# Kernel optimization log

Hardware: AMD Instinct MI355X
Metric: run time of the kernel (lower is better)

Reference implementation:

```python
import jax, jax.numpy as jnp
import numpy as np

GROUP_SIZE = 128
QMAX = 127.0  # int8 symmetric: 2^(8-1) - 1
EPS = 1e-8


def group_quant_dequant(t, group_size=GROUP_SIZE):
    """Group-wise symmetric int8 fake-quantize along the last dim.

    Groups of `group_size` along the last axis share one scale
    s = max|t| / 127; values are rounded/clipped to int8 range and
    immediately dequantized (q * s), which is the exact math of a
    group-quantized GEMM with inline dequantization.
    """
    shape = t.shape
    g = t.reshape(shape[:-1] + (shape[-1] // group_size, group_size))
    s = jnp.maximum(jnp.max(jnp.abs(g), axis=-1, keepdims=True) / QMAX, EPS)
    q = jnp.clip(jnp.round(g / s), -QMAX, QMAX)
    return (q * s).reshape(shape)


def setup_inputs() -> dict:
    key = jax.random.key(0)
    k0, k1, k2, k3 = jax.random.split(key, 4)
    B, S, H, I = 2, 2048, 4096, 11008
    x = jax.random.normal(k0, (B, S, H), dtype=jnp.float32)
    # Linear weights stored [out_features, in_features]; quant groups run
    # along the in_features (contraction) axis.
    w_gate = jax.random.normal(k1, (I, H), dtype=jnp.float32) * (1.0 / np.sqrt(H))
    w_up = jax.random.normal(k2, (I, H), dtype=jnp.float32) * (1.0 / np.sqrt(H))
    w_down = jax.random.normal(k3, (H, I), dtype=jnp.float32) * (1.0 / np.sqrt(I))
    return {"x": x, "w_gate": w_gate, "w_up": w_up, "w_down": w_down}


def reference(x, w_gate, w_up, w_down):
    # quantize input activations (QuantTensor(x))
    xq = group_quant_dequant(x)
    # gate/up quant-GEMMs with inline weight dequant
    gate = jnp.einsum('bsh,ih->bsi', xq, group_quant_dequant(w_gate))
    up = jnp.einsum('bsh,ih->bsi', xq, group_quant_dequant(w_up))
    # SwiGLU: SiLU(gate) * up, then requantize the hidden activation
    hidden = jax.nn.silu(gate) * up
    hq = group_quant_dequant(hidden)
    # down quant-GEMM -> dequantized float output
    out = jnp.einsum('bsi,hi->bsh', hq, group_quant_dequant(w_down))
    return out
```

## Files before the change

### kernel.cpp

```cpp
#include <hip/hip_runtime.h>
#include <math.h>

typedef int i32x4 __attribute__((ext_vector_type(4)));
typedef float f32x4 __attribute__((ext_vector_type(4)));
typedef float f32x2 __attribute__((ext_vector_type(2)));

#define QMAXF 127.0f
#define EPSQ 1e-8f

__device__ __forceinline__ void gl_lds16(const void* g, void* l) {
  __builtin_amdgcn_global_load_lds(
      (const __attribute__((address_space(1))) unsigned int*)g,
      (__attribute__((address_space(3))) unsigned int*)l, 16, 0, 0);
}
__device__ __forceinline__ void gl_lds4(const void* g, void* l) {
  __builtin_amdgcn_global_load_lds(
      (const __attribute__((address_space(1))) unsigned int*)g,
      (__attribute__((address_space(3))) unsigned int*)l, 4, 0, 0);
}

__global__ __launch_bounds__(256)
void qdq8(const float* __restrict__ in, char* __restrict__ q,
          float* __restrict__ sT, long n_groups, int gpr, int R) {
  long wid = (long)blockIdx.x * 4 + (threadIdx.x >> 6);
  if (wid >= n_groups) return;
  int lane = threadIdx.x & 63;
  long base = wid * 128 + lane * 2;
  f32x2 v = *(const f32x2*)(in + base);
  float m = fmaxf(fabsf(v.x), fabsf(v.y));
#pragma unroll
  for (int off = 32; off; off >>= 1) m = fmaxf(m, __shfl_xor(m, off));
  float s = fmaxf(m / QMAXF, EPSQ);
  int q0 = (int)fminf(fmaxf(rintf(v.x / s), -QMAXF), QMAXF);
  int q1 = (int)fminf(fmaxf(rintf(v.y / s), -QMAXF), QMAXF);
  *(unsigned short*)(q + base) =
      (unsigned short)((q0 & 0xff) | ((q1 & 0xff) << 8));
  if (lane == 0) {
    long row = wid / gpr;
    long gc = wid - row * gpr;
    sT[gc * (long)R + row] = s;
  }
}


__global__ __launch_bounds__(256, 2)
void gemm_gu_i8(const char* __restrict__ Aq, const char* __restrict__ Bg,
                const char* __restrict__ Bu,
                const float* __restrict__ sAT, const float* __restrict__ sGT,
                const float* __restrict__ sUT,
                char* __restrict__ Hq, float* __restrict__ sHT,
                int M, int N, int K, int NBN) {
  __shared__ char sA[16384];
  __shared__ char sBG[16384];
  __shared__ char sBU[16384];
  __shared__ float sSa[128], sSg[128], sSu[128];
  __shared__ float rmx[2][128];
  __shared__ float rs[128];

  const int tid = threadIdx.x;
  const int lane = tid & 63;
  const int wid = tid >> 6;
  const int wr = (wid >> 1) * 64;
  const int wc = (wid & 1) * 64;
  const int l15 = lane & 15, l16 = lane >> 4;

  const int nwg = gridDim.x;
  const int wg = ((int)blockIdx.x & 7) * (nwg >> 3) + ((int)blockIdx.x >> 3);
  const long m0 = (long)(wg / NBN) * 128;
  const long n0 = (long)(wg % NBN) * 128;

  const char* gA[4];
  const char* gG[4];
  const char* gU[4];
#pragma unroll
  for (int k = 0; k < 4; k++) {
    int c = tid + 256 * k;
    long row = c >> 3;
    int off = ((c & 7) * 16) ^ ((int)(row & 7) << 4);
    gA[k] = Aq + (m0 + row) * K + off;
    gG[k] = Bg + (n0 + row) * K + off;
    gU[k] = Bu + (n0 + row) * K + off;
  }

  const int rdSwz = (l15 & 7) << 4;
  const int colK0 = (l16 * 16) ^ rdSwz;
  const int colK1 = (64 + l16 * 16) ^ rdSwz;

  f32x4 accg[4][4], accu[4][4];
#pragma unroll
  for (int i = 0; i < 4; i++)
#pragma unroll
    for (int j = 0; j < 4; j++) {
      accg[i][j] = (f32x4){0.f, 0.f, 0.f, 0.f};
      accu[i][j] = (f32x4){0.f, 0.f, 0.f, 0.f};
    }
  const i32x4 iz = {0, 0, 0, 0};

  const int KG = K >> 7;
  for (int g = 0; g < KG; ++g) {
    const long kb = (long)g << 7;
#pragma unroll
    for (int k = 0; k < 4; k++) {
      gl_lds16(gA[k] + kb, &sA[(tid + 256 * k) * 16]);
      gl_lds16(gG[k] + kb, &sBG[(tid + 256 * k) * 16]);
      gl_lds16(gU[k] + kb, &sBU[(tid + 256 * k) * 16]);
    }
    if (wid < 2) {
      gl_lds4(sAT + (long)g * M + m0 + tid, &sSa[wid * 64]);
      gl_lds4(sUT + (long)g * N + n0 + tid, &sSu[wid * 64]);
    } else {
      gl_lds4(sGT + (long)g * N + n0 + (tid - 128), &sSg[(wid - 2) * 64]);
    }
    __syncthreads();

    i32x4 af[4][2];
#pragma unroll
    for (int i = 0; i < 4; i++) {
      const int rb = (wr + i * 16 + l15) * 128;
      af[i][0] = *(const i32x4*)&sA[rb + colK0];
      af[i][1] = *(const i32x4*)&sA[rb + colK1];
    }
    f32x4 sa4[4];
#pragma unroll
    for (int i = 0; i < 4; i++)
      sa4[i] = *(const f32x4*)&sSa[wr + i * 16 + l16 * 4];

#pragma unroll
    for (int j = 0; j < 4; j++) {
      const int rbB = (wc + j * 16 + l15) * 128;
      i32x4 bgf[2], buf_[2];
      bgf[0] = *(const i32x4*)&sBG[rbB + colK0];
      bgf[1] = *(const i32x4*)&sBG[rbB + colK1];
      buf_[0] = *(const i32x4*)&sBU[rbB + colK0];
      buf_[1] = *(const i32x4*)&sBU[rbB + colK1];
      float sbg = sSg[wc + j * 16 + l15];
      float sbu = sSu[wc + j * 16 + l15];
#pragma unroll
      for (int i = 0; i < 4; i++) {
        i32x4 tg = __builtin_amdgcn_mfma_i32_16x16x64_i8(af[i][0], bgf[0], iz, 0, 0, 0);
        tg = __builtin_amdgcn_mfma_i32_16x16x64_i8(af[i][1], bgf[1], tg, 0, 0, 0);
        i32x4 tu = __builtin_amdgcn_mfma_i32_16x16x64_i8(af[i][0], buf_[0], iz, 0, 0, 0);
        tu = __builtin_amdgcn_mfma_i32_16x16x64_i8(af[i][1], buf_[1], tu, 0, 0, 0);
        f32x4 mg = sa4[i] * sbg;
        f32x4 mu = sa4[i] * sbu;
        accg[i][j] += mg * __builtin_convertvector(tg, f32x4);
        accu[i][j] += mu * __builtin_convertvector(tu, f32x4);
      }
    }
    __syncthreads();
  }

  float pm[4][4];
#pragma unroll
  for (int i = 0; i < 4; i++)
#pragma unroll
    for (int r = 0; r < 4; r++) pm[i][r] = 0.f;
#pragma unroll
  for (int i = 0; i < 4; i++)
#pragma unroll
    for (int j = 0; j < 4; j++)
#pragma unroll
      for (int r = 0; r < 4; r++) {
        float gv = accg[i][j][r];
        float h = gv / (1.f + expf(-gv)) * accu[i][j][r];
        accu[i][j][r] = h;
        pm[i][r] = fmaxf(pm[i][r], fabsf(h));
      }
#pragma unroll
  for (int i = 0; i < 4; i++)
#pragma unroll
    for (int r = 0; r < 4; r++) {
      pm[i][r] = fmaxf(pm[i][r], __shfl_xor(pm[i][r], 1));
      pm[i][r] = fmaxf(pm[i][r], __shfl_xor(pm[i][r], 2));
      pm[i][r] = fmaxf(pm[i][r], __shfl_xor(pm[i][r], 4));
      pm[i][r] = fmaxf(pm[i][r], __shfl_xor(pm[i][r], 8));
    }
#pragma unroll
  for (int i = 0; i < 4; i++)
#pragma unroll
    for (int r = 0; r < 4; r++)
      if (l15 == i * 4 + r) rmx[wid & 1][wr + i * 16 + l16 * 4 + r] = pm[i][r];
  __syncthreads();
  if (tid < 128) {
    float mx = fmaxf(rmx[0][tid], rmx[1][tid]);
    float s = fmaxf(mx / QMAXF, EPSQ);
    rs[tid] = s;
    sHT[(n0 >> 7) * (long)M + m0 + tid] = s;
  }
  __syncthreads();
#pragma unroll
  for (int i = 0; i < 4; i++) {
    f32x4 sr = *(const f32x4*)&rs[wr + i * 16 + l16 * 4];
#pragma unroll
    for (int j = 0; j < 4; j++)
#pragma unroll
      for (int r = 0; r < 4; r++) {
        float qv = fminf(fmaxf(rintf(accu[i][j][r] / sr[r]), -QMAXF), QMAXF);
        sA[(wr + i * 16 + l16 * 4 + r) * 128 + wc + j * 16 + l15] = (char)(int)qv;
      }
  }
  __syncthreads();
  {
    int row = tid >> 1, seg = tid & 1;
    const i32x4* src = (const i32x4*)&sA[row * 128 + seg * 64];
    i32x4* dst = (i32x4*)(Hq + (m0 + row) * N + n0 + seg * 64);
#pragma unroll
    for (int k = 0; k < 4; k++) dst[k] = src[k];
  }
}

__global__ __launch_bounds__(256, 2)
void gemm_dn_i8(const char* __restrict__ Aq, const char* __restrict__ Bq,
                const float* __restrict__ sAT, const float* __restrict__ sBT,
                float* __restrict__ C, int M, int N, int K, int NBN) {
  __shared__ char sA[16384];
  __shared__ char sB[16384];
  __shared__ float sSa[128], sSb[128];

  const int tid = threadIdx.x;
  const int lane = tid & 63;
  const int wid = tid >> 6;
  const int wr = (wid >> 1) * 64;
  const int wc = (wid & 1) * 64;
  const int l15 = lane & 15, l16 = lane >> 4;

  const int nwg = gridDim.x;
  const int wg = ((int)blockIdx.x & 7) * (nwg >> 3) + ((int)blockIdx.x >> 3);
  const long m0 = (long)(wg / NBN) * 128;
  const long n0 = (long)(wg % NBN) * 128;

  const char* gA[4];
  const char* gB[4];
#pragma unroll
  for (int k = 0; k < 4; k++) {
    int c = tid + 256 * k;
    long row = c >> 3;
    int off = ((c & 7) * 16) ^ ((int)(row & 7) << 4);
    gA[k] = Aq + (m0 + row) * K + off;
    gB[k] = Bq + (n0 + row) * K + off;
  }

  const int rdSwz = (l15 & 7) << 4;
  const int colK0 = (l16 * 16) ^ rdSwz;
  const int colK1 = (64 + l16 * 16) ^ rdSwz;

  f32x4 acc[4][4];
#pragma unroll
  for (int i = 0; i < 4; i++)
#pragma unroll
    for (int j = 0; j < 4; j++) acc[i][j] = (f32x4){0.f, 0.f, 0.f, 0.f};
  const i32x4 iz = {0, 0, 0, 0};

  const int KG = K >> 7;
  for (int g = 0; g < KG; ++g) {
    const long kb = (long)g << 7;
#pragma unroll
    for (int k = 0; k < 4; k++) {
      gl_lds16(gA[k] + kb, &sA[(tid + 256 * k) * 16]);
      gl_lds16(gB[k] + kb, &sB[(tid + 256 * k) * 16]);
    }
    if (wid < 2) {
      gl_lds4(sAT + (long)g * M + m0 + tid, &sSa[wid * 64]);
    } else {
      gl_lds4(sBT + (long)g * N + n0 + (tid - 128), &sSb[(wid - 2) * 64]);
    }
    __syncthreads();

    i32x4 af[4][2];
#pragma unroll
    for (int i = 0; i < 4; i++) {
      const int rb = (wr + i * 16 + l15) * 128;
      af[i][0] = *(const i32x4*)&sA[rb + colK0];
      af[i][1] = *(const i32x4*)&sA[rb + colK1];
    }
    f32x4 sa4[4];
#pragma unroll
    for (int i = 0; i < 4; i++)
      sa4[i] = *(const f32x4*)&sSa[wr + i * 16 + l16 * 4];

#pragma unroll
    for (int j = 0; j < 4; j++) {
      const int rbB = (wc + j * 16 + l15) * 128;
      i32x4 bf[2];
      bf[0] = *(const i32x4*)&sB[rbB + colK0];
      bf[1] = *(const i32x4*)&sB[rbB + colK1];
      float sb = sSb[wc + j * 16 + l15];
#pragma unroll
      for (int i = 0; i < 4; i++) {
        i32x4 t = __builtin_amdgcn_mfma_i32_16x16x64_i8(af[i][0], bf[0], iz, 0, 0, 0);
        t = __builtin_amdgcn_mfma_i32_16x16x64_i8(af[i][1], bf[1], t, 0, 0, 0);
        f32x4 ms = sa4[i] * sb;
        acc[i][j] += ms * __builtin_convertvector(t, f32x4);
      }
    }
    __syncthreads();
  }

#pragma unroll
  for (int i = 0; i < 4; i++)
#pragma unroll
    for (int j = 0; j < 4; j++)
#pragma unroll
      for (int r = 0; r < 4; r++) {
        long row = m0 + wr + i * 16 + l16 * 4 + r;
        long col = n0 + wc + j * 16 + l15;
        C[row * N + col] = acc[i][j][r];
      }
}

extern "C" void kernel_launch(void* const* d_in, const int* in_sizes, int n_in,
                              void* d_out, int out_size, void* d_ws, size_t ws_size,
                              hipStream_t stream) {
  (void)n_in; (void)out_size;
  const float* x  = (const float*)d_in[0];
  const float* wg = (const float*)d_in[1];
  const float* wu = (const float*)d_in[2];
  const float* wd = (const float*)d_in[3];
  float* out = (float*)d_out;

  const long H = 4096;
  const long M = in_sizes[0] / H;
  const long I = in_sizes[1] / H;
  const long GH = H >> 7;
  const long GI = I >> 7;

  char* ws = (char*)d_ws;
  size_t off = 0;
  char* xq  = ws + off; off += (size_t)(M * H);
  char* wgq = ws + off; off += (size_t)(I * H);
  char* wuq = ws + off; off += (size_t)(I * H);
  char* wdq = ws + off; off += (size_t)(H * I);
  char* hq  = ws + off; off += (size_t)(M * I);
  float* s_x = (float*)(ws + off); off += (size_t)(GH * M) * 4;
  float* s_g = (float*)(ws + off); off += (size_t)(GH * I) * 4;
  float* s_u = (float*)(ws + off); off += (size_t)(GH * I) * 4;
  float* s_d = (float*)(ws + off); off += (size_t)(GI * H) * 4;
  float* s_h = (float*)(ws + off); off += (size_t)(GI * M) * 4;
  if (ws_size < off) return;

  {
    long ng;
    ng = M * H / 128;
    qdq8<<<dim3((unsigned)((ng + 3) / 4)), dim3(256), 0, stream>>>(x, xq, s_x, ng, (int)GH, (int)M);
    ng = I * H / 128;
    qdq8<<<dim3((unsigned)((ng + 3) / 4)), dim3(256), 0, stream>>>(wg, wgq, s_g, ng, (int)GH, (int)I);
    qdq8<<<dim3((unsigned)((ng + 3) / 4)), dim3(256), 0, stream>>>(wu, wuq, s_u, ng, (int)GH, (int)I);
    ng = H * I / 128;
    qdq8<<<dim3((unsigned)((ng + 3) / 4)), dim3(256), 0, stream>>>(wd, wdq, s_d, ng, (int)GI, (int)H);
  }

  {
    const int NBN = (int)GI;
    const int grid = (int)(M / 128) * NBN;
    gemm_gu_i8<<<dim3(grid), dim3(256), 0, stream>>>(
        xq, wgq, wuq, s_x, s_g, s_u, hq, s_h, (int)M, (int)I, (int)H, NBN);
  }
  {
    const int NBN = (int)GH;
    const int grid = (int)(M / 128) * NBN;
    gemm_dn_i8<<<dim3(grid), dim3(256), 0, stream>>>(
        hq, wdq, s_h, s_d, out, (int)M, (int)H, (int)I, NBN);
  }
}
```

Measured before the change: 1.172 ms.

## Prefetch next K-tile into LDS during MFMA compute in int8 GEMMs

Restructures both int8 GEMM main loops so the next K-group's global-to-LDS loads are issued right after the current fragments are read into registers. The MFMA work then overlaps with those loads, and the gate/up kernel splits the B loads so the up-weight tile is refetched only after its fragments have been consumed. Launch bounds drop to one block per SIMD to leave room for the larger register-resident fragments. The cost is lower occupancy and extra barriers per iteration.

```diff
diff --git a/kernel.cpp b/kernel.cpp
--- a/kernel.cpp
+++ b/kernel.cpp
@@ -43,7 +43,7 @@
 }
 
 
-__global__ __launch_bounds__(256, 2)
+__global__ __launch_bounds__(256, 1)
 void gemm_gu_i8(const char* __restrict__ Aq, const char* __restrict__ Bg,
                 const char* __restrict__ Bu,
                 const float* __restrict__ sAT, const float* __restrict__ sGT,
@@ -69,17 +69,24 @@
   const long m0 = (long)(wg / NBN) * 128;
   const long n0 = (long)(wg % NBN) * 128;
 
-  const char* gA[4];
-  const char* gG[4];
-  const char* gU[4];
-#pragma unroll
-  for (int k = 0; k < 4; k++) {
-    int c = tid + 256 * k;
-    long row = c >> 3;
-    int off = ((c & 7) * 16) ^ ((int)(row & 7) << 4);
-    gA[k] = Aq + (m0 + row) * K + off;
-    gG[k] = Bg + (n0 + row) * K + off;
-    gU[k] = Bu + (n0 + row) * K + off;
+  const long row0 = tid >> 3;
+  const int off0 = (((tid & 7) * 16)) ^ ((int)(row0 & 7) << 4);
+  const long kstr = 32L * K;
+  const char* gA0 = Aq + (m0 + row0) * K + off0;
+  const char* gG0 = Bg + (n0 + row0) * K + off0;
+  const char* gU0 = Bu + (n0 + row0) * K + off0;
+
+  const float* pS0;
+  const float* pS1;
+  float* dS0;
+  float* dS1;
+  long st0 = 0, st1 = 0;
+  if (wid < 2) {
+    pS0 = sAT + m0 + tid; dS0 = &sSa[wid * 64]; st0 = M;
+    pS1 = sUT + n0 + tid; dS1 = &sSu[wid * 64]; st1 = N;
+  } else {
+    pS0 = sGT + n0 + (tid - 128); dS0 = &sSg[(wid - 2) * 64]; st0 = N;
+    pS1 = pS0; dS1 = dS0;
   }
 
   const int rdSwz = (l15 & 7) << 4;
@@ -95,58 +102,87 @@
       accu[i][j] = (f32x4){0.f, 0.f, 0.f, 0.f};
     }
   const i32x4 iz = {0, 0, 0, 0};
-
   const int KG = K >> 7;
+
+#pragma unroll
+  for (int k = 0; k < 4; k++) {
+    gl_lds16(gA0 + k * kstr, &sA[tid * 16 + k * 4096]);
+    gl_lds16(gG0 + k * kstr, &sBG[tid * 16 + k * 4096]);
+    gl_lds16(gU0 + k * kstr, &sBU[tid * 16 + k * 4096]);
+  }
+  gA0 += 128; gG0 += 128; gU0 += 128;
+  gl_lds4(pS0, dS0); pS0 += st0;
+  if (wid < 2) { gl_lds4(pS1, dS1); pS1 += st1; }
+  asm volatile("s_waitcnt vmcnt(0)" ::: "memory");
+  __syncthreads();
+
   for (int g = 0; g < KG; ++g) {
-    const long kb = (long)g << 7;
-#pragma unroll
-    for (int k = 0; k < 4; k++) {
-      gl_lds16(gA[k] + kb, &sA[(tid + 256 * k) * 16]);
-      gl_lds16(gG[k] + kb, &sBG[(tid + 256 * k) * 16]);
-      gl_lds16(gU[k] + kb, &sBU[(tid + 256 * k) * 16]);
-    }
-    if (wid < 2) {
-      gl_lds4(sAT + (long)g * M + m0 + tid, &sSa[wid * 64]);
-      gl_lds4(sUT + (long)g * N + n0 + tid, &sSu[wid * 64]);
-    } else {
-      gl_lds4(sGT + (long)g * N + n0 + (tid - 128), &sSg[(wid - 2) * 64]);
-    }
-    __syncthreads();
-
-    i32x4 af[4][2];
+    const bool pf = (g + 1 < KG);
+    i32x4 af[4][2], bgf[4][2];
 #pragma unroll
     for (int i = 0; i < 4; i++) {
       const int rb = (wr + i * 16 + l15) * 128;
       af[i][0] = *(const i32x4*)&sA[rb + colK0];
       af[i][1] = *(const i32x4*)&sA[rb + colK1];
     }
+#pragma unroll
+    for (int j = 0; j < 4; j++) {
+      const int rb = (wc + j * 16 + l15) * 128;
+      bgf[j][0] = *(const i32x4*)&sBG[rb + colK0];
+      bgf[j][1] = *(const i32x4*)&sBG[rb + colK1];
+    }
     f32x4 sa4[4];
 #pragma unroll
     for (int i = 0; i < 4; i++)
       sa4[i] = *(const f32x4*)&sSa[wr + i * 16 + l16 * 4];
-
+    f32x4 sbg4, sbu4;
 #pragma unroll
     for (int j = 0; j < 4; j++) {
-      const int rbB = (wc + j * 16 + l15) * 128;
-      i32x4 bgf[2], buf_[2];
-      bgf[0] = *(const i32x4*)&sBG[rbB + colK0];
-      bgf[1] = *(const i32x4*)&sBG[rbB + colK1];
-      buf_[0] = *(const i32x4*)&sBU[rbB + colK0];
-      buf_[1] = *(const i32x4*)&sBU[rbB + colK1];
-      float sbg = sSg[wc + j * 16 + l15];
-      float sbu = sSu[wc + j * 16 + l15];
+      sbg4[j] = sSg[wc + j * 16 + l15];
+      sbu4[j] = sSu[wc + j * 16 + l15];
+    }
+    __syncthreads();
+    if (pf) {
+#pragma unroll
+      for (int k = 0; k < 4; k++) {
+        gl_lds16(gA0 + k * kstr, &sA[tid * 16 + k * 4096]);
+        gl_lds16(gG0 + k * kstr, &sBG[tid * 16 + k * 4096]);
+      }
+      gA0 += 128; gG0 += 128;
+      gl_lds4(pS0, dS0); pS0 += st0;
+      if (wid < 2) { gl_lds4(pS1, dS1); pS1 += st1; }
+    }
+#pragma unroll
+    for (int j = 0; j < 4; j++)
 #pragma unroll
       for (int i = 0; i < 4; i++) {
-        i32x4 tg = __builtin_amdgcn_mfma_i32_16x16x64_i8(af[i][0], bgf[0], iz, 0, 0, 0);
-        tg = __builtin_amdgcn_mfma_i32_16x16x64_i8(af[i][1], bgf[1], tg, 0, 0, 0);
-        i32x4 tu = __builtin_amdgcn_mfma_i32_16x16x64_i8(af[i][0], buf_[0], iz, 0, 0, 0);
-        tu = __builtin_amdgcn_mfma_i32_16x16x64_i8(af[i][1], buf_[1], tu, 0, 0, 0);
-        f32x4 mg = sa4[i] * sbg;
-        f32x4 mu = sa4[i] * sbu;
-        accg[i][j] += mg * __builtin_convertvector(tg, f32x4);
-        accu[i][j] += mu * __builtin_convertvector(tu, f32x4);
-      }
-    }
+        i32x4 tg = __builtin_amdgcn_mfma_i32_16x16x64_i8(af[i][0], bgf[j][0], iz, 0, 0, 0);
+        tg = __builtin_amdgcn_mfma_i32_16x16x64_i8(af[i][1], bgf[j][1], tg, 0, 0, 0);
+        accg[i][j] += (sa4[i] * sbg4[j]) * __builtin_convertvector(tg, f32x4);
+      }
+    i32x4 buf_[4][2];
+#pragma unroll
+    for (int j = 0; j < 4; j++) {
+      const int rb = (wc + j * 16 + l15) * 128;
+      buf_[j][0] = *(const i32x4*)&sBU[rb + colK0];
+      buf_[j][1] = *(const i32x4*)&sBU[rb + colK1];
+    }
+    __syncthreads();
+    if (pf) {
+#pragma unroll
+      for (int k = 0; k < 4; k++)
+        gl_lds16(gU0 + k * kstr, &sBU[tid * 16 + k * 4096]);
+      gU0 += 128;
+    }
+#pragma unroll
+    for (int j = 0; j < 4; j++)
+#pragma unroll
+      for (int i = 0; i < 4; i++) {
+        i32x4 tu = __builtin_amdgcn_mfma_i32_16x16x64_i8(af[i][0], buf_[j][0], iz, 0, 0, 0);
+        tu = __builtin_amdgcn_mfma_i32_16x16x64_i8(af[i][1], buf_[j][1], tu, 0, 0, 0);
+        accu[i][j] += (sa4[i] * sbu4[j]) * __builtin_convertvector(tu, f32x4);
+      }
+    asm volatile("s_waitcnt vmcnt(0)" ::: "memory");
     __syncthreads();
   }
 
@@ -209,7 +245,7 @@
   }
 }
 
-__global__ __launch_bounds__(256, 2)
+__global__ __launch_bounds__(256, 1)
 void gemm_dn_i8(const char* __restrict__ Aq, const char* __restrict__ Bq,
                 const float* __restrict__ sAT, const float* __restrict__ sBT,
                 float* __restrict__ C, int M, int N, int K, int NBN) {
@@ -229,15 +265,19 @@
   const long m0 = (long)(wg / NBN) * 128;
   const long n0 = (long)(wg % NBN) * 128;
 
-  const char* gA[4];
-  const char* gB[4];
-#pragma unroll
-  for (int k = 0; k < 4; k++) {
-    int c = tid + 256 * k;
-    long row = c >> 3;
-    int off = ((c & 7) * 16) ^ ((int)(row & 7) << 4);
-    gA[k] = Aq + (m0 + row) * K + off;
-    gB[k] = Bq + (n0 + row) * K + off;
+  const long row0 = tid >> 3;
+  const int off0 = (((tid & 7) * 16)) ^ ((int)(row0 & 7) << 4);
+  const long kstr = 32L * K;
+  const char* gA0 = Aq + (m0 + row0) * K + off0;
+  const char* gB0 = Bq + (n0 + row0) * K + off0;
+
+  const float* pS0;
+  float* dS0;
+  long st0;
+  if (wid < 2) {
+    pS0 = sAT + m0 + tid; dS0 = &sSa[wid * 64]; st0 = M;
+  } else {
+    pS0 = sBT + n0 + (tid - 128); dS0 = &sSb[(wid - 2) * 64]; st0 = N;
   }
 
   const int rdSwz = (l15 & 7) << 4;
@@ -250,49 +290,59 @@
 #pragma unroll
     for (int j = 0; j < 4; j++) acc[i][j] = (f32x4){0.f, 0.f, 0.f, 0.f};
   const i32x4 iz = {0, 0, 0, 0};
-
   const int KG = K >> 7;
+
+#pragma unroll
+  for (int k = 0; k < 4; k++) {
+    gl_lds16(gA0 + k * kstr, &sA[tid * 16 + k * 4096]);
+    gl_lds16(gB0 + k * kstr, &sB[tid * 16 + k * 4096]);
+  }
+  gA0 += 128; gB0 += 128;
+  gl_lds4(pS0, dS0); pS0 += st0;
+  asm volatile("s_waitcnt vmcnt(0)" ::: "memory");
+  __syncthreads();
+
   for (int g = 0; g < KG; ++g) {
-    const long kb = (long)g << 7;
-#pragma unroll
-    for (int k = 0; k < 4; k++) {
-      gl_lds16(gA[k] + kb, &sA[(tid + 256 * k) * 16]);
-      gl_lds16(gB[k] + kb, &sB[(tid + 256 * k) * 16]);
-    }
-    if (wid < 2) {
-      gl_lds4(sAT + (long)g * M + m0 + tid, &sSa[wid * 64]);
-    } else {
-      gl_lds4(sBT + (long)g * N + n0 + (tid - 128), &sSb[(wid - 2) * 64]);
-    }
-    __syncthreads();
-
-    i32x4 af[4][2];
+    const bool pf = (g + 1 < KG);
+    i32x4 af[4][2], bf[4][2];
 #pragma unroll
     for (int i = 0; i < 4; i++) {
       const int rb = (wr + i * 16 + l15) * 128;
       af[i][0] = *(const i32x4*)&sA[rb + colK0];
       af[i][1] = *(const i32x4*)&sA[rb + colK1];
     }
+#pragma unroll
+    for (int j = 0; j < 4; j++) {
+      const int rb = (wc + j * 16 + l15) * 128;
+      bf[j][0] = *(const i32x4*)&sB[rb + colK0];
+      bf[j][1] = *(const i32x4*)&sB[rb + colK1];
+    }
     f32x4 sa4[4];
 #pragma unroll
     for (int i = 0; i < 4; i++)
       sa4[i] = *(const f32x4*)&sSa[wr + i * 16 + l16 * 4];
-
-#pragma unroll
-    for (int j = 0; j < 4; j++) {
-      const int rbB = (wc + j * 16 + l15) * 128;
-      i32x4 bf[2];
-      bf[0] = *(const i32x4*)&sB[rbB + colK0];
-      bf[1] = *(const i32x4*)&sB[rbB + colK1];
-      float sb = sSb[wc + j * 16 + l15];
+    f32x4 sb4;
+#pragma unroll
+    for (int j = 0; j < 4; j++) sb4[j] = sSb[wc + j * 16 + l15];
+    __syncthreads();
+    if (pf) {
+#pragma unroll
+      for (int k = 0; k < 4; k++) {
+        gl_lds16(gA0 + k * kstr, &sA[tid * 16 + k * 4096]);
+        gl_lds16(gB0 + k * kstr, &sB[tid * 16 + k * 4096]);
+      }
+      gA0 += 128; gB0 += 128;
+      gl_lds4(pS0, dS0); pS0 += st0;
+    }
+#pragma unroll
+    for (int j = 0; j < 4; j++)
 #pragma unroll
       for (int i = 0; i < 4; i++) {
-        i32x4 t = __builtin_amdgcn_mfma_i32_16x16x64_i8(af[i][0], bf[0], iz, 0, 0, 0);
-        t = __builtin_amdgcn_mfma_i32_16x16x64_i8(af[i][1], bf[1], t, 0, 0, 0);
-        f32x4 ms = sa4[i] * sb;
-        acc[i][j] += ms * __builtin_convertvector(t, f32x4);
-      }
-    }
+        i32x4 t = __builtin_amdgcn_mfma_i32_16x16x64_i8(af[i][0], bf[j][0], iz, 0, 0, 0);
+        t = __builtin_amdgcn_mfma_i32_16x16x64_i8(af[i][1], bf[j][1], t, 0, 0, 0);
+        acc[i][j] += (sa4[i] * sb4[j]) * __builtin_convertvector(t, f32x4);
+      }
+    asm volatile("s_waitcnt vmcnt(0)" ::: "memory");
     __syncthreads();
   }
 
```

After: 1.449 ms. 1.24x slower.
